# Optimization experiments

Measured on AMD Instinct MI355X. Metric: run time of the kernel, lower is better.

The kernel has to match this reference:

```python
import jax, jax.numpy as jnp
import numpy as np

N, E, D = 50000, 600000, 128
NEG_SLOPE = 0.2

def setup_inputs() -> dict:
    key = jax.random.key(0)
    ks = jax.random.split(key, 12)
    s = 1.0 / np.sqrt(D)
    return {
        "x": jax.random.normal(ks[0], (N, D), jnp.float32),
        "edge_index": jax.random.randint(ks[1], (2, E), 0, N),
        "edge_attr": jax.random.normal(ks[2], (E, D), jnp.float32),
        "ln1_g": jnp.ones((D,), jnp.float32),
        "ln1_b": jnp.zeros((D,), jnp.float32),
        "W_lin": jax.random.normal(ks[3], (D, D), jnp.float32) * s,
        "att_src": jax.random.normal(ks[4], (D,), jnp.float32) * s,
        "att_dst": jax.random.normal(ks[5], (D,), jnp.float32) * s,
        "W_edge": jax.random.normal(ks[6], (D, D), jnp.float32) * s,
        "att_edge": jax.random.normal(ks[7], (D,), jnp.float32) * s,
        "gat_bias": jnp.zeros((D,), jnp.float32),
        "ln2_g": jnp.ones((D,), jnp.float32),
        "ln2_b": jnp.zeros((D,), jnp.float32),
        "W1": jax.random.normal(ks[8], (D, 4 * D), jnp.float32) * s,
        "b1": jnp.zeros((4 * D,), jnp.float32),
        "W2": jax.random.normal(ks[9], (4 * D, D), jnp.float32) * (1.0 / np.sqrt(4 * D)),
        "b2": jnp.zeros((D,), jnp.float32),
    }


def _layernorm(x, g, b, eps=1e-5):
    mu = jnp.mean(x, axis=-1, keepdims=True)
    var = jnp.mean(jnp.square(x - mu), axis=-1, keepdims=True)
    return (x - mu) * jax.lax.rsqrt(var + eps) * g + b


def _gat_conv(x, edge_index, edge_attr, W_lin, att_src, att_dst, W_edge, att_edge, gat_bias):
    # PyG GATConv, heads=1, concat=False, add_self_loops=False, edge_dim=D
    src, dst = edge_index[0], edge_index[1]
    h = x @ W_lin                      # [N, D] shared src/dst projection
    a_src = h @ att_src                # [N]
    a_dst = h @ att_dst                # [N]
    a_edge = (edge_attr @ W_edge) @ att_edge  # [E]
    alpha = a_src[src] + a_dst[dst] + a_edge  # [E]
    alpha = jnp.where(alpha > 0, alpha, NEG_SLOPE * alpha)  # leaky_relu(0.2)
    # segment softmax over destination nodes
    m = jax.ops.segment_max(alpha, dst, num_segments=N)
    m = jnp.where(jnp.isfinite(m), m, 0.0)
    ex = jnp.exp(alpha - m[dst])
    denom = jax.ops.segment_sum(ex, dst, num_segments=N)
    coef = ex / jnp.maximum(denom[dst], 1e-16)
    # weighted scatter-aggregation of source messages
    out = jax.ops.segment_sum(coef[:, None] * h[src], dst, num_segments=N)
    return out + gat_bias


def reference(x, edge_index, edge_attr, ln1_g, ln1_b, W_lin, att_src, att_dst,
              W_edge, att_edge, gat_bias, ln2_g, ln2_b, W1, b1, W2, b2):
    # pre-norm + GAT message passing + residual (dropout = eval identity)
    xn = _layernorm(x, ln1_g, ln1_b)
    x = x + _gat_conv(xn, edge_index, edge_attr, W_lin, att_src, att_dst,
                      W_edge, att_edge, gat_bias)
    # pre-norm + FFN + residual
    xn = _layernorm(x, ln2_g, ln2_b)
    ffn = jax.nn.relu(xn @ W1 + b1) @ W2 + b2
    return x + ffn
```

## Files before the change

kernel.cpp:

```cpp
#include <hip/hip_runtime.h>

#define D 128
#define NEG_SLOPE 0.2f

typedef __attribute__((ext_vector_type(8))) short short8;
typedef __attribute__((ext_vector_type(4))) float f32x4;

__device__ __forceinline__ float wred_sum(float v){
#pragma unroll
  for (int m = 32; m; m >>= 1) v += __shfl_xor(v, m);
  return v;
}
__device__ __forceinline__ int wred_sumi(int v){
#pragma unroll
  for (int m = 32; m; m >>= 1) v += __shfl_xor(v, m);
  return v;
}
__device__ __forceinline__ float wred_max(float v){
#pragma unroll
  for (int m = 32; m; m >>= 1) v = fmaxf(v, __shfl_xor(v, m));
  return v;
}
__device__ __forceinline__ unsigned short bf16r(float f){
  unsigned int u = __float_as_uint(f);
  u += 0x7fffu + ((u >> 16) & 1u);
  return (unsigned short)(u >> 16);
}
__device__ __forceinline__ float bf2f(unsigned int hi16){
  return __uint_as_float(hi16 << 16);
}

__global__ void k_ln1(const float* __restrict__ x, const float* __restrict__ g,
                      const float* __restrict__ b, unsigned short* __restrict__ xnq,
                      int* __restrict__ cnt, int N){
  int gid = blockIdx.x * blockDim.x + threadIdx.x;
  if (gid < N) cnt[gid] = 0;
  int w = gid >> 6;
  int lane = threadIdx.x & 63;
  if (w >= N) return;
  float2 v = *(const float2*)(x + (size_t)w * D + lane * 2);
  float mu = wred_sum(v.x + v.y) * (1.0f / D);
  float d0 = v.x - mu, d1 = v.y - mu;
  float var = wred_sum(d0 * d0 + d1 * d1) * (1.0f / D);
  float rstd = rsqrtf(var + 1e-5f);
  float2 gv = *(const float2*)(g + lane * 2);
  float2 bv = *(const float2*)(b + lane * 2);
  float o0 = d0 * rstd * gv.x + bv.x;
  float o1 = d1 * rstd * gv.y + bv.y;
  unsigned int p = (unsigned int)bf16r(o0) | ((unsigned int)bf16r(o1) << 16);
  *(unsigned int*)(xnq + (size_t)w * D + lane * 2) = p;
}

__global__ void k_prep(const float* __restrict__ W_lin, const float* __restrict__ W1,
                       const float* __restrict__ W2, const float* __restrict__ W_edge,
                       const float* __restrict__ att_edge, const int* __restrict__ ei,
                       unsigned short* __restrict__ Wlt, unsigned short* __restrict__ W1t,
                       unsigned short* __restrict__ W2t, float* __restrict__ we,
                       int* __restrict__ cnt, int E){
  int t = blockIdx.x * blockDim.x + threadIdx.x;
  if (t < 128 * 128){
    int c = t >> 7, k = t & 127;
    Wlt[t] = bf16r(W_lin[k * 128 + c]);
  } else if (t < 128 * 128 + 512 * 128){
    int u = t - 128 * 128; int c = u >> 7, k = u & 127;
    W1t[u] = bf16r(W1[k * 512 + c]);
  } else if (t < 128 * 128 + 512 * 128 + 128 * 512){
    int u = t - (128 * 128 + 512 * 128); int c = u >> 9, k = u & 511;
    W2t[u] = bf16r(W2[k * 128 + c]);
  } else {
    int u = t - (128 * 128 + 512 * 128 + 128 * 512);
    if (u < 128){
      float s = 0.f;
      for (int j = 0; j < 128; ++j) s += W_edge[u * 128 + j] * att_edge[j];
      we[u] = s;
    }
  }
  int stride = gridDim.x * blockDim.x;
  for (int e = t; e < E; e += stride) atomicAdd(&cnt[ei[E + e]], 1);
}

__global__ __launch_bounds__(256) void k_hgemm(const unsigned short* __restrict__ xnq,
                                               const unsigned short* __restrict__ Wlt,
                                               const float* __restrict__ att_src,
                                               const float* __restrict__ att_dst,
                                               unsigned short* __restrict__ hq,
                                               float* __restrict__ asrc,
                                               float* __restrict__ adst, int N){
  int wid = threadIdx.x >> 6, lane = threadIdx.x & 63;
  int rb = blockIdx.x * 64 + wid * 16;
  int row = rb + (lane & 15);
  int rowc = row < N ? row : N - 1;
  int ksub = (lane >> 4) * 8;
  short8 a[4];
#pragma unroll
  for (int kb = 0; kb < 4; ++kb)
    a[kb] = *(const short8*)(xnq + (size_t)rowc * 128 + kb * 32 + ksub);
  f32x4 acc[8];
#pragma unroll
  for (int ct = 0; ct < 8; ++ct) acc[ct] = (f32x4){0.f, 0.f, 0.f, 0.f};
#pragma unroll
  for (int ct = 0; ct < 8; ++ct){
    int col = ct * 16 + (lane & 15);
#pragma unroll
    for (int kb = 0; kb < 4; ++kb){
      short8 bf = *(const short8*)(Wlt + (size_t)col * 128 + kb * 32 + ksub);
      acc[ct] = __builtin_amdgcn_mfma_f32_16x16x32_bf16(a[kb], bf, acc[ct], 0, 0, 0);
    }
  }
  int r0 = rb + (lane >> 4) * 4;
#pragma unroll
  for (int ct = 0; ct < 8; ++ct){
    int col = ct * 16 + (lane & 15);
#pragma unroll
    for (int j = 0; j < 4; ++j){
      int r = r0 + j;
      if (r < N) hq[(size_t)r * 128 + col] = bf16r(acc[ct][j]);
    }
  }
  float as_v[8], ad_v[8];
#pragma unroll
  for (int ct = 0; ct < 8; ++ct){
    int col = ct * 16 + (lane & 15);
    as_v[ct] = att_src[col];
    ad_v[ct] = att_dst[col];
  }
  float ps[4] = {0.f, 0.f, 0.f, 0.f}, pd[4] = {0.f, 0.f, 0.f, 0.f};
#pragma unroll
  for (int ct = 0; ct < 8; ++ct)
#pragma unroll
    for (int j = 0; j < 4; ++j){
      ps[j] += acc[ct][j] * as_v[ct];
      pd[j] += acc[ct][j] * ad_v[ct];
    }
#pragma unroll
  for (int m = 1; m < 16; m <<= 1)
#pragma unroll
    for (int j = 0; j < 4; ++j){
      ps[j] += __shfl_xor(ps[j], m);
      pd[j] += __shfl_xor(pd[j], m);
    }
  if ((lane & 15) == 0){
#pragma unroll
    for (int j = 0; j < 4; ++j){
      int r = r0 + j;
      if (r < N){ asrc[r] = ps[j]; adst[r] = pd[j]; }
    }
  }
}

__global__ void k_bsum(const int* __restrict__ cnt, int* __restrict__ bsum, int N){
  int t = threadIdx.x;
  int i = blockIdx.x * 256 + t;
  int v = (i < N) ? cnt[i] : 0;
  v = wred_sumi(v);
  __shared__ int ws[4];
  if ((t & 63) == 0) ws[t >> 6] = v;
  __syncthreads();
  if (t == 0) bsum[blockIdx.x] = ws[0] + ws[1] + ws[2] + ws[3];
}

__global__ void k_escan(const int* __restrict__ cnt, const int* __restrict__ bsum,
                        int* __restrict__ start, int* __restrict__ cursor, int N){
  int b = blockIdx.x, t = threadIdx.x;
  __shared__ int s_off;
  if (t < 64){
    int acc = 0;
    for (int j = t; j < b; j += 64) acc += bsum[j];
    acc = wred_sumi(acc);
    if (t == 0) s_off = acc;
  }
  int i = b * 256 + t;
  int c = (i < N) ? cnt[i] : 0;
  __shared__ int sd[256];
  sd[t] = c;
  __syncthreads();
  for (int off = 1; off < 256; off <<= 1){
    int v = (t >= off) ? sd[t - off] : 0;
    __syncthreads();
    sd[t] += v;
    __syncthreads();
  }
  int st = s_off + sd[t] - c;
  if (i <= N) start[i] = st;
  if (i < N) cursor[i] = st;
}

__global__ void k_edge_scatter(const float* __restrict__ ea, const int* __restrict__ ei,
                               const float* __restrict__ we, const float* __restrict__ asrc,
                               const float* __restrict__ adst, int* __restrict__ cursor,
                               int2* __restrict__ esa, int E){
  int gw = (blockIdx.x * blockDim.x + threadIdx.x) >> 6;
  int lane = threadIdx.x & 63;
  int e = gw * 2 + (lane >> 5);
  int li = lane & 31;
  if (e >= E) return;
  float4 v = *(const float4*)(ea + (size_t)e * 128 + li * 4);
  float4 w = *(const float4*)(we + li * 4);
  float s = v.x * w.x + v.y * w.y + v.z * w.z + v.w * w.w;
#pragma unroll
  for (int m = 16; m; m >>= 1) s += __shfl_xor(s, m);
  if (li == 0){
    int sn = ei[e], dn = ei[E + e];
    float al = asrc[sn] + adst[dn] + s;
    al = al > 0.f ? al : NEG_SLOPE * al;
    int slot = atomicAdd(&cursor[dn], 1);
    esa[slot] = make_int2(sn, __float_as_int(al));
  }
}

__global__ void k_agg(const float* __restrict__ x, const unsigned short* __restrict__ hq,
                      const int* __restrict__ start, const int2* __restrict__ esa,
                      const float* __restrict__ gat_bias,
                      const float* __restrict__ g2, const float* __restrict__ b2,
                      float* __restrict__ out, unsigned short* __restrict__ xn2q, int N){
  int n = (blockIdx.x * blockDim.x + threadIdx.x) >> 6;
  int lane = threadIdx.x & 63;
  if (n >= N) return;
  int beg = start[n], end = start[n + 1];
  float m = -1e30f;
  for (int i = beg + lane; i < end; i += 64) m = fmaxf(m, __int_as_float(esa[i].y));
  m = wred_max(m);
  float ds = 0.f, a0 = 0.f, a1 = 0.f;
#pragma unroll 2
  for (int s = beg; s < end; ++s){
    int2 ev = esa[s];
    float ex = __expf(__int_as_float(ev.y) - m);
    ds += ex;
    unsigned int hv = *(const unsigned int*)(hq + (size_t)ev.x * 128 + lane * 2);
    a0 += ex * bf2f(hv & 0xffffu);
    a1 += ex * bf2f(hv >> 16);
  }
  float inv = (end > beg) ? 1.f / fmaxf(ds, 1e-16f) : 0.f;
  a0 *= inv; a1 *= inv;
  float2 xv  = *(const float2*)(x + (size_t)n * 128 + lane * 2);
  float2 gbv = *(const float2*)(gat_bias + lane * 2);
  float r0 = xv.x + a0 + gbv.x;
  float r1 = xv.y + a1 + gbv.y;
  float mu = wred_sum(r0 + r1) * (1.0f / 128.f);
  float d0 = r0 - mu, d1 = r1 - mu;
  float var = wred_sum(d0 * d0 + d1 * d1) * (1.0f / 128.f);
  float rstd = rsqrtf(var + 1e-5f);
  float2 gv = *(const float2*)(g2 + lane * 2);
  float2 bv = *(const float2*)(b2 + lane * 2);
  float o0 = d0 * rstd * gv.x + bv.x;
  float o1 = d1 * rstd * gv.y + bv.y;
  *(float2*)(out + (size_t)n * 128 + lane * 2) = make_float2(r0, r1);
  unsigned int p = (unsigned int)bf16r(o0) | ((unsigned int)bf16r(o1) << 16);
  *(unsigned int*)(xn2q + (size_t)n * 128 + lane * 2) = p;
}

__global__ __launch_bounds__(512) void k_ffn(const unsigned short* __restrict__ xn2q,
                                             const unsigned short* __restrict__ W1t,
                                             const unsigned short* __restrict__ W2t,
                                             const float* __restrict__ b1,
                                             const float* __restrict__ b2,
                                             float* __restrict__ out, int N){
  __shared__ unsigned short hid[64 * 512];
  int wid = threadIdx.x >> 6, lane = threadIdx.x & 63;
  int rg = wid >> 1;
  int ch = wid & 1;
  int rb = blockIdx.x * 64;
  int lr = rg * 16;
  int arow = rb + lr + (lane & 15);
  int arowc = arow < N ? arow : N - 1;
  int ksub = (lane >> 4) * 8;
  short8 a[4];
#pragma unroll
  for (int kb = 0; kb < 4; ++kb)
    a[kb] = *(const short8*)(xn2q + (size_t)arowc * 128 + kb * 32 + ksub);
  int lr0 = lr + (lane >> 4) * 4;
#pragma unroll 4
  for (int ct = 0; ct < 16; ++ct){
    int col = ch * 256 + ct * 16 + (lane & 15);
    f32x4 acc = {0.f, 0.f, 0.f, 0.f};
#pragma unroll
    for (int kb = 0; kb < 4; ++kb){
      short8 bf = *(const short8*)(W1t + (size_t)col * 128 + kb * 32 + ksub);
      acc = __builtin_amdgcn_mfma_f32_16x16x32_bf16(a[kb], bf, acc, 0, 0, 0);
    }
    float bias = b1[col];
#pragma unroll
    for (int j = 0; j < 4; ++j){
      float v = acc[j] + bias;
      v = v > 0.f ? v : 0.f;
      int row = lr0 + j;
      int byte = (col * 2) ^ ((row & 7) << 4);
      *(unsigned short*)((char*)hid + row * 1024 + byte) = bf16r(v);
    }
  }
  __syncthreads();
  f32x4 acc2[4];
#pragma unroll
  for (int ct = 0; ct < 4; ++ct) acc2[ct] = (f32x4){0.f, 0.f, 0.f, 0.f};
  int arow2 = lr + (lane & 15);
#pragma unroll 2
  for (int kb = 0; kb < 16; ++kb){
    int kbyte = (kb * 32 + ksub) * 2;
    int sb = kbyte ^ ((arow2 & 7) << 4);
    short8 af = *(const short8*)((const char*)hid + arow2 * 1024 + sb);
#pragma unroll
    for (int ct = 0; ct < 4; ++ct){
      int col = ch * 64 + ct * 16 + (lane & 15);
      short8 bf = *(const short8*)(W2t + (size_t)col * 512 + kb * 32 + ksub);
      acc2[ct] = __builtin_amdgcn_mfma_f32_16x16x32_bf16(af, bf, acc2[ct], 0, 0, 0);
    }
  }
  int r0 = rb + lr0;
#pragma unroll
  for (int ct = 0; ct < 4; ++ct){
    int col = ch * 64 + ct * 16 + (lane & 15);
    float bias = b2[col];
#pragma unroll
    for (int j = 0; j < 4; ++j){
      int row = r0 + j;
      if (row < N) out[(size_t)row * 128 + col] += acc2[ct][j] + bias;
    }
  }
}

extern "C" void kernel_launch(void* const* d_in, const int* in_sizes, int n_in,
                              void* d_out, int out_size, void* d_ws, size_t ws_size,
                              hipStream_t stream){
  const float* x        = (const float*)d_in[0];
  const int*   ei       = (const int*)  d_in[1];
  const float* ea       = (const float*)d_in[2];
  const float* ln1_g    = (const float*)d_in[3];
  const float* ln1_b    = (const float*)d_in[4];
  const float* W_lin    = (const float*)d_in[5];
  const float* att_src  = (const float*)d_in[6];
  const float* att_dst  = (const float*)d_in[7];
  const float* W_edge   = (const float*)d_in[8];
  const float* att_edge = (const float*)d_in[9];
  const float* gat_bias = (const float*)d_in[10];
  const float* ln2_g    = (const float*)d_in[11];
  const float* ln2_b    = (const float*)d_in[12];
  const float* W1       = (const float*)d_in[13];
  const float* b1       = (const float*)d_in[14];
  const float* W2       = (const float*)d_in[15];
  const float* b2       = (const float*)d_in[16];

  const int N = in_sizes[0] / 128;
  const int E = in_sizes[2] / 128;
  const int NB = (N + 255) / 256;
  float* out = (float*)d_out;

  char* p = (char*)d_ws;
  auto carve = [&](size_t bytes) -> char* {
    char* r = p; p += (bytes + 255) & ~(size_t)255; return r;
  };
  unsigned short* xnq      = (unsigned short*)carve((size_t)N * 128 * 2);
  unsigned short* hq       = (unsigned short*)carve((size_t)N * 128 * 2);
  float*          asrc     = (float*)carve((size_t)N * 4);
  float*          adst     = (float*)carve((size_t)N * 4);
  int2*           esa      = (int2*)carve((size_t)E * 8);
  int*            cnt      = (int*)carve((size_t)N * 4);
  int*            cursor   = (int*)carve((size_t)N * 4);
  int*            start    = (int*)carve((size_t)(N + 1) * 4);
  int*            bsum     = (int*)carve((size_t)NB * 4);
  unsigned short* Wlt      = (unsigned short*)carve(128 * 128 * 2);
  unsigned short* W1t      = (unsigned short*)carve(512 * 128 * 2);
  unsigned short* W2t      = (unsigned short*)carve(128 * 512 * 2);
  float*          we       = (float*)carve(128 * 4);
  unsigned short* xn2q     = xnq;

  int nwb = (N + 3) / 4;
  k_ln1<<<nwb, 256, 0, stream>>>(x, ln1_g, ln1_b, xnq, cnt, N);
  k_prep<<<(E + 255) / 256, 256, 0, stream>>>(W_lin, W1, W2, W_edge, att_edge, ei,
                                              Wlt, W1t, W2t, we, cnt, E);
  k_hgemm<<<(N + 63) / 64, 256, 0, stream>>>(xnq, Wlt, att_src, att_dst, hq, asrc, adst, N);
  k_bsum<<<NB, 256, 0, stream>>>(cnt, bsum, N);
  k_escan<<<NB, 256, 0, stream>>>(cnt, bsum, start, cursor, N);
  k_edge_scatter<<<(E + 7) / 8, 256, 0, stream>>>(ea, ei, we, asrc, adst, cursor, esa, E);
  k_agg<<<nwb, 256, 0, stream>>>(x, hq, start, esa, gat_bias, ln2_g, ln2_b, out, xn2q, N);
  k_ffn<<<(N + 63) / 64, 512, 0, stream>>>(xn2q, W1t, W2t, b1, b2, out, N);
}
```

Measured before the change: 344.4 us.

## Fuse LN1 into projection GEMM, merge scan kernels, batch gathers in aggregation

LayerNorm-1 is now computed inside the projection GEMM kernel from the fp32 input, so the bf16 intermediate buffer and the separate LN kernel go away. The edge in-degree histogram moves into the tail of the GEMM kernel, and the two-pass block-sum plus scan is merged into one scan kernel in which each block re-sums all preceding counts itself. The aggregation kernel switches to an online softmax that loads 64 edges per wave at once and broadcasts them with shuffles, issuing four independent row gathers per iteration to raise memory-level parallelism. The trade-offs are a quadratic-ish redundant prefix read in the scan and more register use in the GEMM.

```diff
diff --git a/kernel.cpp b/kernel.cpp
--- a/kernel.cpp
+++ b/kernel.cpp
@@ -30,34 +30,14 @@
   return __uint_as_float(hi16 << 16);
 }
 
-__global__ void k_ln1(const float* __restrict__ x, const float* __restrict__ g,
-                      const float* __restrict__ b, unsigned short* __restrict__ xnq,
-                      int* __restrict__ cnt, int N){
-  int gid = blockIdx.x * blockDim.x + threadIdx.x;
-  if (gid < N) cnt[gid] = 0;
-  int w = gid >> 6;
-  int lane = threadIdx.x & 63;
-  if (w >= N) return;
-  float2 v = *(const float2*)(x + (size_t)w * D + lane * 2);
-  float mu = wred_sum(v.x + v.y) * (1.0f / D);
-  float d0 = v.x - mu, d1 = v.y - mu;
-  float var = wred_sum(d0 * d0 + d1 * d1) * (1.0f / D);
-  float rstd = rsqrtf(var + 1e-5f);
-  float2 gv = *(const float2*)(g + lane * 2);
-  float2 bv = *(const float2*)(b + lane * 2);
-  float o0 = d0 * rstd * gv.x + bv.x;
-  float o1 = d1 * rstd * gv.y + bv.y;
-  unsigned int p = (unsigned int)bf16r(o0) | ((unsigned int)bf16r(o1) << 16);
-  *(unsigned int*)(xnq + (size_t)w * D + lane * 2) = p;
-}
-
-__global__ void k_prep(const float* __restrict__ W_lin, const float* __restrict__ W1,
-                       const float* __restrict__ W2, const float* __restrict__ W_edge,
-                       const float* __restrict__ att_edge, const int* __restrict__ ei,
-                       unsigned short* __restrict__ Wlt, unsigned short* __restrict__ W1t,
-                       unsigned short* __restrict__ W2t, float* __restrict__ we,
-                       int* __restrict__ cnt, int E){
+__global__ void k_prep0(const float* __restrict__ W_lin, const float* __restrict__ W1,
+                        const float* __restrict__ W2, const float* __restrict__ W_edge,
+                        const float* __restrict__ att_edge,
+                        unsigned short* __restrict__ Wlt, unsigned short* __restrict__ W1t,
+                        unsigned short* __restrict__ W2t, float* __restrict__ we,
+                        int* __restrict__ cnt, int N){
   int t = blockIdx.x * blockDim.x + threadIdx.x;
+  if (t < N) cnt[t] = 0;
   if (t < 128 * 128){
     int c = t >> 7, k = t & 127;
     Wlt[t] = bf16r(W_lin[k * 128 + c]);
@@ -75,26 +55,59 @@
       we[u] = s;
     }
   }
-  int stride = gridDim.x * blockDim.x;
-  for (int e = t; e < E; e += stride) atomicAdd(&cnt[ei[E + e]], 1);
-}
-
-__global__ __launch_bounds__(256) void k_hgemm(const unsigned short* __restrict__ xnq,
+}
+
+__global__ __launch_bounds__(256) void k_hgemm(const float* __restrict__ x,
                                                const unsigned short* __restrict__ Wlt,
+                                               const float* __restrict__ ln1_g,
+                                               const float* __restrict__ ln1_b,
                                                const float* __restrict__ att_src,
                                                const float* __restrict__ att_dst,
+                                               const int* __restrict__ ei,
                                                unsigned short* __restrict__ hq,
                                                float* __restrict__ asrc,
-                                               float* __restrict__ adst, int N){
+                                               float* __restrict__ adst,
+                                               int* __restrict__ cnt, int N, int E){
   int wid = threadIdx.x >> 6, lane = threadIdx.x & 63;
   int rb = blockIdx.x * 64 + wid * 16;
   int row = rb + (lane & 15);
   int rowc = row < N ? row : N - 1;
   int ksub = (lane >> 4) * 8;
+  float v[4][8];
+#pragma unroll
+  for (int kb = 0; kb < 4; ++kb){
+    float4 p0 = *(const float4*)(x + (size_t)rowc * 128 + kb * 32 + ksub);
+    float4 p1 = *(const float4*)(x + (size_t)rowc * 128 + kb * 32 + ksub + 4);
+    v[kb][0] = p0.x; v[kb][1] = p0.y; v[kb][2] = p0.z; v[kb][3] = p0.w;
+    v[kb][4] = p1.x; v[kb][5] = p1.y; v[kb][6] = p1.z; v[kb][7] = p1.w;
+  }
+  float s = 0.f;
+#pragma unroll
+  for (int kb = 0; kb < 4; ++kb)
+#pragma unroll
+    for (int j = 0; j < 8; ++j) s += v[kb][j];
+  s += __shfl_xor(s, 16); s += __shfl_xor(s, 32);
+  float mu = s * (1.0f / 128.f);
+  float q = 0.f;
+#pragma unroll
+  for (int kb = 0; kb < 4; ++kb)
+#pragma unroll
+    for (int j = 0; j < 8; ++j){ float d = v[kb][j] - mu; q += d * d; }
+  q += __shfl_xor(q, 16); q += __shfl_xor(q, 32);
+  float rstd = rsqrtf(q * (1.0f / 128.f) + 1e-5f);
   short8 a[4];
 #pragma unroll
-  for (int kb = 0; kb < 4; ++kb)
-    a[kb] = *(const short8*)(xnq + (size_t)rowc * 128 + kb * 32 + ksub);
+  for (int kb = 0; kb < 4; ++kb){
+    float4 g0 = *(const float4*)(ln1_g + kb * 32 + ksub);
+    float4 g1 = *(const float4*)(ln1_g + kb * 32 + ksub + 4);
+    float4 b0 = *(const float4*)(ln1_b + kb * 32 + ksub);
+    float4 b1 = *(const float4*)(ln1_b + kb * 32 + ksub + 4);
+    float gg[8] = {g0.x,g0.y,g0.z,g0.w,g1.x,g1.y,g1.z,g1.w};
+    float bb[8] = {b0.x,b0.y,b0.z,b0.w,b1.x,b1.y,b1.z,b1.w};
+#pragma unroll
+    for (int j = 0; j < 8; ++j)
+      a[kb][j] = (short)bf16r((v[kb][j] - mu) * rstd * gg[j] + bb[j]);
+  }
   f32x4 acc[8];
 #pragma unroll
   for (int ct = 0; ct < 8; ++ct) acc[ct] = (f32x4){0.f, 0.f, 0.f, 0.f};
@@ -146,38 +159,31 @@
       if (r < N){ asrc[r] = ps[j]; adst[r] = pd[j]; }
     }
   }
-}
-
-__global__ void k_bsum(const int* __restrict__ cnt, int* __restrict__ bsum, int N){
-  int t = threadIdx.x;
-  int i = blockIdx.x * 256 + t;
-  int v = (i < N) ? cnt[i] : 0;
-  v = wred_sumi(v);
-  __shared__ int ws[4];
-  if ((t & 63) == 0) ws[t >> 6] = v;
+  int t = blockIdx.x * blockDim.x + threadIdx.x;
+  int stride = gridDim.x * blockDim.x;
+  for (int e = t; e < E; e += stride) atomicAdd(&cnt[ei[E + e]], 1);
+}
+
+__global__ void k_escan(const int* __restrict__ cnt, int* __restrict__ start,
+                        int* __restrict__ cursor, int N){
+  int b = blockIdx.x, t = threadIdx.x;
+  int base = b * 256;
+  int acc = 0;
+  for (int i = t; i < base; i += 256) acc += cnt[i];
+  acc = wred_sumi(acc);
+  __shared__ int wsum[4];
+  if ((t & 63) == 0) wsum[t >> 6] = acc;
   __syncthreads();
-  if (t == 0) bsum[blockIdx.x] = ws[0] + ws[1] + ws[2] + ws[3];
-}
-
-__global__ void k_escan(const int* __restrict__ cnt, const int* __restrict__ bsum,
-                        int* __restrict__ start, int* __restrict__ cursor, int N){
-  int b = blockIdx.x, t = threadIdx.x;
-  __shared__ int s_off;
-  if (t < 64){
-    int acc = 0;
-    for (int j = t; j < b; j += 64) acc += bsum[j];
-    acc = wred_sumi(acc);
-    if (t == 0) s_off = acc;
-  }
-  int i = b * 256 + t;
+  int s_off = wsum[0] + wsum[1] + wsum[2] + wsum[3];
+  int i = base + t;
   int c = (i < N) ? cnt[i] : 0;
   __shared__ int sd[256];
   sd[t] = c;
   __syncthreads();
   for (int off = 1; off < 256; off <<= 1){
-    int v = (t >= off) ? sd[t - off] : 0;
+    int vv = (t >= off) ? sd[t - off] : 0;
     __syncthreads();
-    sd[t] += v;
+    sd[t] += vv;
     __syncthreads();
   }
   int st = s_off + sd[t] - c;
@@ -217,18 +223,40 @@
   int lane = threadIdx.x & 63;
   if (n >= N) return;
   int beg = start[n], end = start[n + 1];
-  float m = -1e30f;
-  for (int i = beg + lane; i < end; i += 64) m = fmaxf(m, __int_as_float(esa[i].y));
-  m = wred_max(m);
-  float ds = 0.f, a0 = 0.f, a1 = 0.f;
-#pragma unroll 2
-  for (int s = beg; s < end; ++s){
-    int2 ev = esa[s];
-    float ex = __expf(__int_as_float(ev.y) - m);
-    ds += ex;
-    unsigned int hv = *(const unsigned int*)(hq + (size_t)ev.x * 128 + lane * 2);
-    a0 += ex * bf2f(hv & 0xffffu);
-    a1 += ex * bf2f(hv >> 16);
+  float m = -1e30f, ds = 0.f, a0 = 0.f, a1 = 0.f;
+  for (int cb = beg; cb < end; cb += 64){
+    int k = end - cb; if (k > 64) k = 64;
+    int2 ev = (cb + lane < end) ? esa[cb + lane] : make_int2(0, (int)0xFF800000u);
+    float al = __int_as_float(ev.y);
+    float mn = fmaxf(m, wred_max(al));
+    float sc = __expf(m - mn);
+    ds *= sc; a0 *= sc; a1 *= sc;
+    m = mn;
+    float ex = __expf(al - m);
+    int j = 0;
+    for (; j + 4 <= k; j += 4){
+      float e0 = __shfl(ex, j), e1 = __shfl(ex, j + 1);
+      float e2 = __shfl(ex, j + 2), e3 = __shfl(ex, j + 3);
+      int s0 = __shfl(ev.x, j), s1 = __shfl(ev.x, j + 1);
+      int s2 = __shfl(ev.x, j + 2), s3 = __shfl(ev.x, j + 3);
+      unsigned int h0 = *(const unsigned int*)(hq + (size_t)s0 * 128 + lane * 2);
+      unsigned int h1 = *(const unsigned int*)(hq + (size_t)s1 * 128 + lane * 2);
+      unsigned int h2 = *(const unsigned int*)(hq + (size_t)s2 * 128 + lane * 2);
+      unsigned int h3 = *(const unsigned int*)(hq + (size_t)s3 * 128 + lane * 2);
+      ds += e0 + e1 + e2 + e3;
+      a0 += e0 * bf2f(h0 & 0xffffu) + e1 * bf2f(h1 & 0xffffu)
+          + e2 * bf2f(h2 & 0xffffu) + e3 * bf2f(h3 & 0xffffu);
+      a1 += e0 * bf2f(h0 >> 16) + e1 * bf2f(h1 >> 16)
+          + e2 * bf2f(h2 >> 16) + e3 * bf2f(h3 >> 16);
+    }
+    for (; j < k; ++j){
+      float ej = __shfl(ex, j);
+      int sj = __shfl(ev.x, j);
+      unsigned int hv = *(const unsigned int*)(hq + (size_t)sj * 128 + lane * 2);
+      ds += ej;
+      a0 += ej * bf2f(hv & 0xffffu);
+      a1 += ej * bf2f(hv >> 16);
+    }
   }
   float inv = (end > beg) ? 1.f / fmaxf(ds, 1e-16f) : 0.f;
   a0 *= inv; a1 *= inv;
@@ -341,36 +369,32 @@
 
   const int N = in_sizes[0] / 128;
   const int E = in_sizes[2] / 128;
-  const int NB = (N + 255) / 256;
   float* out = (float*)d_out;
 
   char* p = (char*)d_ws;
   auto carve = [&](size_t bytes) -> char* {
     char* r = p; p += (bytes + 255) & ~(size_t)255; return r;
   };
-  unsigned short* xnq      = (unsigned short*)carve((size_t)N * 128 * 2);
   unsigned short* hq       = (unsigned short*)carve((size_t)N * 128 * 2);
+  unsigned short* xn2q     = (unsigned short*)carve((size_t)N * 128 * 2);
   float*          asrc     = (float*)carve((size_t)N * 4);
   float*          adst     = (float*)carve((size_t)N * 4);
   int2*           esa      = (int2*)carve((size_t)E * 8);
   int*            cnt      = (int*)carve((size_t)N * 4);
   int*            cursor   = (int*)carve((size_t)N * 4);
   int*            start    = (int*)carve((size_t)(N + 1) * 4);
-  int*            bsum     = (int*)carve((size_t)NB * 4);
   unsigned short* Wlt      = (unsigned short*)carve(128 * 128 * 2);
   unsigned short* W1t      = (unsigned short*)carve(512 * 128 * 2);
   unsigned short* W2t      = (unsigned short*)carve(128 * 512 * 2);
   float*          we       = (float*)carve(128 * 4);
-  unsigned short* xn2q     = xnq;
-
-  int nwb = (N + 3) / 4;
-  k_ln1<<<nwb, 256, 0, stream>>>(x, ln1_g, ln1_b, xnq, cnt, N);
-  k_prep<<<(E + 255) / 256, 256, 0, stream>>>(W_lin, W1, W2, W_edge, att_edge, ei,
-                                              Wlt, W1t, W2t, we, cnt, E);
-  k_hgemm<<<(N + 63) / 64, 256, 0, stream>>>(xnq, Wlt, att_src, att_dst, hq, asrc, adst, N);
-  k_bsum<<<NB, 256, 0, stream>>>(cnt, bsum, N);
-  k_escan<<<NB, 256, 0, stream>>>(cnt, bsum, start, cursor, N);
+
+  k_prep0<<<(128*128 + 512*128 + 128*512 + 128 + 255) / 256, 256, 0, stream>>>(
+      W_lin, W1, W2, W_edge, att_edge, Wlt, W1t, W2t, we, cnt, N);
+  k_hgemm<<<(N + 63) / 64, 256, 0, stream>>>(x, Wlt, ln1_g, ln1_b, att_src, att_dst, ei,
+                                             hq, asrc, adst, cnt, N, E);
+  k_escan<<<N / 256 + 1, 256, 0, stream>>>(cnt, start, cursor, N);
   k_edge_scatter<<<(E + 7) / 8, 256, 0, stream>>>(ea, ei, we, asrc, adst, cursor, esa, E);
-  k_agg<<<nwb, 256, 0, stream>>>(x, hq, start, esa, gat_bias, ln2_g, ln2_b, out, xn2q, N);
+  k_agg<<<(N + 3) / 4, 256, 0, stream>>>(x, hq, start, esa, gat_bias, ln2_g, ln2_b,
+                                         out, xn2q, N);
   k_ffn<<<(N + 63) / 64, 512, 0, stream>>>(xn2q, W1t, W2t, b1, b2, out, N);
 }
```

Result: no change. 344.9 us (+0.2%).
